# Kernel optimization log

Hardware: AMD Instinct MI355X
Metric: run time of the kernel (lower is better)

Reference implementation:

```python
import jax, jax.numpy as jnp
import numpy as np

ALPHA = 0.5            # conf['alpha'] hybrid mixing
MAX_TOP_ANT = 50       # conf['max_top_antecedents']
MAX_SPAN_WIDTH = 30


def bucket_distance(d):
    # util.bucket_distance: identity 0..4, then log2 buckets, clipped to [0, 9]
    logspace = jnp.floor(jnp.log2(jnp.maximum(d, 1).astype(jnp.float32))).astype(d.dtype) + 3
    return jnp.clip(jnp.where(d <= 4, d, logspace), 0, 9)


def setup_inputs() -> dict:
    key = jax.random.key(0)
    ks = jax.random.split(key, 16)
    W, D, K, F, H = 4096, 768, 768, 20, 1000
    SPAN = 3 * D                      # span_emb_size = 3 * bert_emb_size
    PAIR = 3 * SPAN + F               # pair_emb_size (use_features only)
    std = 0.02

    mention_doc = jax.random.normal(ks[0], (W, D), jnp.float32)
    mention_doc_one = jax.random.normal(ks[1], (W, D), jnp.float32)
    top_span_starts = jnp.sort(jax.random.randint(ks[2], (K,), 0, W - MAX_SPAN_WIDTH))
    widths = jax.random.randint(ks[3], (K,), 0, MAX_SPAN_WIDTH)
    top_span_ends = jnp.minimum(top_span_starts + widths, W - 1)
    top_span_mention_scores = jax.random.normal(ks[4], (K,), jnp.float32)

    return {
        "mention_doc": mention_doc,
        "mention_doc_one": mention_doc_one,
        "top_span_starts": top_span_starts,
        "top_span_ends": top_span_ends,
        "top_span_mention_scores": top_span_mention_scores,
        # mention_token_attn: Linear(D -> 1)
        "attn_w": jax.random.normal(ks[5], (D,), jnp.float32) * std,
        "attn_b": jnp.zeros((), jnp.float32),
        # coarse_bilinear: Linear(SPAN -> SPAN)
        "coarse_w": jax.random.normal(ks[6], (SPAN, SPAN), jnp.float32) * std,
        "coarse_b": jnp.zeros((SPAN,), jnp.float32),
        # emb_antecedent_distance_prior [10, F] + antecedent_distance_score_ffnn Linear(F -> 1)
        "dist_prior_emb": jax.random.normal(ks[7], (10, F), jnp.float32) * std,
        "dist_w": jax.random.normal(ks[8], (F,), jnp.float32) * std,
        "dist_b": jnp.zeros((), jnp.float32),
        # emb_top_antecedent_distance [10, F]
        "top_dist_emb": jax.random.normal(ks[9], (10, F), jnp.float32) * std,
        # coref_score_ffnn: Linear(PAIR -> H), ReLU, Linear(H -> 1)
        "coref_w1": jax.random.normal(ks[10], (PAIR, H), jnp.float32) * std,
        "coref_b1": jnp.zeros((H,), jnp.float32),
        "coref_w2": jax.random.normal(ks[11], (H,), jnp.float32) * std,
        "coref_b2": jnp.zeros((), jnp.float32),
    }


def reference(mention_doc, mention_doc_one, top_span_starts, top_span_ends,
              top_span_mention_scores, attn_w, attn_b, coarse_w, coarse_b,
              dist_prior_emb, dist_w, dist_b, top_dist_emb,
              coref_w1, coref_b1, coref_w2, coref_b2):
    W = mention_doc.shape[0]
    K = top_span_starts.shape[0]
    C = min(K, MAX_TOP_ANT)
    NEG_INF = jnp.float32(-1e30) * 0 - jnp.inf  # true -inf, matches torch.log(0.)

    # --- span embeddings: start / end / head-attention over hybrid doc ---
    start_emb = mention_doc[top_span_starts]                      # [K, D]
    end_emb = mention_doc[top_span_ends]                          # [K, D]
    hybrid = mention_doc * (1.0 - ALPHA) + mention_doc_one * ALPHA
    token_attn = hybrid @ attn_w + attn_b                         # [W]
    tok = jnp.arange(W)
    span_tok_mask = (tok[None, :] >= top_span_starts[:, None]) & \
                    (tok[None, :] <= top_span_ends[:, None])      # [K, W]
    attn_raw = jnp.where(span_tok_mask, token_attn[None, :], NEG_INF)
    attn_probs = jax.nn.softmax(attn_raw, axis=1)                 # [K, W]
    head_emb = attn_probs @ hybrid                                # [K, D]
    span_emb = jnp.concatenate([start_emb, end_emb, head_emb], axis=1)  # [K, 3D]

    # --- coarse (fast) pairwise scores ---
    rng = jnp.arange(K)
    ant_offsets = rng[:, None] - rng[None, :]                     # [K, K]
    ant_mask = ant_offsets >= 1
    pair_sum = top_span_mention_scores[:, None] + top_span_mention_scores[None, :]
    src = span_emb @ coarse_w + coarse_b                          # coarse_bilinear
    fast = pair_sum + src @ span_emb.T
    fast = jnp.where(ant_mask, fast, NEG_INF)                     # + log(mask)
    dist_score = dist_prior_emb @ dist_w + dist_b                 # [10]
    fast = fast + dist_score[bucket_distance(ant_offsets)]        # distance prior

    # --- top-k antecedent pruning ---
    top_fast, top_idx = jax.lax.top_k(fast, C)                    # [K, C]
    top_ant_offsets = jnp.take_along_axis(ant_offsets, top_idx, axis=1)

    # --- fine-grained pairwise FFNN scoring ---
    dist_emb = top_dist_emb[bucket_distance(top_ant_offsets)]     # [K, C, F]
    ant_emb = span_emb[top_idx]                                   # [K, C, 3D]
    tgt_emb = jnp.broadcast_to(span_emb[:, None, :], ant_emb.shape)
    sim_emb = span_emb[:, None, :] * ant_emb
    pair_emb = jnp.concatenate([tgt_emb, ant_emb, sim_emb, dist_emb], axis=-1)  # [K, C, PAIR]
    h = jax.nn.relu(jnp.einsum('kcp,ph->kch', pair_emb, coref_w1) + coref_b1)
    slow = jnp.einsum('kch,h->kc', h, coref_w2) + coref_b2        # [K, C]
    top_scores = slow + top_fast

    # dummy antecedent (epsilon) column of zeros
    return jnp.concatenate([jnp.zeros((K, 1), top_scores.dtype), top_scores], axis=1)
```

## Files before the change

kernel.cpp:

```cpp
#include <hip/hip_runtime.h>
#include <math.h>

#define WTOK 4096
#define DD   768
#define KK   768
#define SPAN 2304
#define HH   1000
#define CC   50
#define NPAD 1024
#define NBIG 4352

typedef __attribute__((ext_vector_type(8))) short bf16x8;
typedef __attribute__((ext_vector_type(4))) float f32x4;
typedef unsigned short ushort;
typedef unsigned int uint;

__device__ __forceinline__ int bucketd(int d) {
  int l = (d >= 1) ? (31 - __clz(d)) : 0;
  int v = (d <= 4) ? d : (l + 3);
  return min(max(v, 0), 9);
}
__device__ __forceinline__ ushort f2bf(float f) {
  uint u = __float_as_uint(f);
  return (ushort)((u + 0x7fffu + ((u >> 16) & 1u)) >> 16);
}
__device__ __forceinline__ uint pkmul_t(uint a, uint b) {
  float lo = __uint_as_float(a << 16) * __uint_as_float(b << 16);
  float hi = __uint_as_float(a & 0xffff0000u) * __uint_as_float(b & 0xffff0000u);
  return __builtin_amdgcn_perm(__float_as_uint(hi), __float_as_uint(lo), 0x07060302u);
}
__device__ __forceinline__ uint4 pkmul4(uint4 a, uint4 b) {
  uint4 r;
  r.x = pkmul_t(a.x, b.x); r.y = pkmul_t(a.y, b.y);
  r.z = pkmul_t(a.z, b.z); r.w = pkmul_t(a.w, b.w);
  return r;
}
__device__ __forceinline__ void dma16(const ushort* g, ushort* l) {
  __builtin_amdgcn_global_load_lds(
      (const __attribute__((address_space(1))) void*)g,
      (__attribute__((address_space(3))) void*)l, 16, 0, 0);
}

#define PB_COARSE 5184
#define PB_W 2304
#define PB_SETUP_BASE (PB_COARSE + 3 * PB_W)
#define PB_SLOW_BASE  (PB_SETUP_BASE + 40)
#define PB_TOTAL      (PB_SLOW_BASE + 150)

__global__ __launch_bounds__(256) void prep_k(
    const float* __restrict__ coarse_w, const float* __restrict__ W1,
    const float* __restrict__ dist_prior, const float* __restrict__ dist_w,
    const float* __restrict__ dist_b, const float* __restrict__ top_dist,
    ushort* __restrict__ BigT, ushort* __restrict__ W1simT,
    float* __restrict__ dist_score, float* __restrict__ Pdist,
    float* __restrict__ slow)
{
  int bid = blockIdx.x;
  int tid = threadIdx.x;
  if (bid >= PB_SLOW_BASE) {
    int t = (bid - PB_SLOW_BASE) * 256 + tid;
    if (t < KK * CC) slow[t] = 0.f;
    return;
  }
  if (bid >= PB_SETUP_BASE) {
    int t = (bid - PB_SETUP_BASE) * 256 + tid;
    if (t < 10) {
      float s = dist_b[0];
      for (int f = 0; f < 20; ++f) s += dist_prior[t * 20 + f] * dist_w[f];
      dist_score[t] = s;
    }
    if (t < 10 * HH) {
      int b = t / HH, h = t % HH;
      float s = 0.f;
      for (int f = 0; f < 20; ++f)
        s += top_dist[b * 20 + f] * W1[(long)(6912 + f) * HH + h];
      Pdist[t] = s;
    }
    return;
  }
  const float* in; int ldin, Cin, nbase, NBrows; ushort* out; int idx;
  int xt;
  if (bid < PB_COARSE) {
    idx = bid; in = coarse_w; ldin = SPAN; Cin = SPAN; nbase = 0;
    NBrows = NBIG; out = BigT; xt = SPAN / 32;
  } else {
    idx = bid - PB_COARSE;
    int region = idx / PB_W;
    idx = idx % PB_W;
    if (region == 0) { in = W1; nbase = 2304; NBrows = NBIG; out = BigT; }
    else if (region == 1) { in = W1 + (size_t)SPAN * HH; nbase = 3328; NBrows = NBIG; out = BigT; }
    else { in = W1 + (size_t)2 * SPAN * HH; nbase = 0; NBrows = NPAD; out = W1simT; }
    ldin = HH; Cin = HH; xt = NPAD / 32;
  }
  {
    int bx = idx % xt, by = idx / xt;
    __shared__ float tile[32][33];
    int n0 = bx * 32, p0 = by * 32;
    int tx = tid & 31, ty = tid >> 5;
    for (int i = ty; i < 32; i += 8) {
      int p = p0 + i, n = n0 + tx;
      tile[i][tx] = (n < Cin) ? in[(long)p * ldin + n] : 0.f;
    }
    __syncthreads();
    size_t slab = (size_t)(p0 >> 5) * NBrows * 32;
    for (int i = ty; i < 32; i += 8) {
      int n = n0 + i;
      out[slab + (size_t)(nbase + n) * 32 + tx] = f2bf(tile[tx][i]);
    }
  }
}

__global__ __launch_bounds__(256) void hybrid_attn_k(
    const float* __restrict__ doc, const float* __restrict__ doc1,
    const float* __restrict__ attn_w, const float* __restrict__ attn_b,
    float* __restrict__ hybrid, float* __restrict__ tok_attn)
{
  int w = blockIdx.x;
  int tid = threadIdx.x;
  float part = 0.f;
  for (int d = tid; d < DD; d += 256) {
    float h = 0.5f * doc[(long)w * DD + d] + 0.5f * doc1[(long)w * DD + d];
    hybrid[(long)w * DD + d] = h;
    part += h * attn_w[d];
  }
  for (int off = 32; off > 0; off >>= 1) part += __shfl_down(part, off, 64);
  __shared__ float ws4[4];
  if ((tid & 63) == 0) ws4[tid >> 6] = part;
  __syncthreads();
  if (tid == 0) tok_attn[w] = ws4[0] + ws4[1] + ws4[2] + ws4[3] + attn_b[0];
}

__global__ __launch_bounds__(256) void span_emb_k(
    const float* __restrict__ doc, const float* __restrict__ hybrid,
    const float* __restrict__ tok_attn, const int* __restrict__ starts,
    const int* __restrict__ ends, ushort* __restrict__ se_bf)
{
  int k = blockIdx.x;
  int s = starts[k], e = ends[k];
  int len = e - s + 1;
  int tid = threadIdx.x;
  __shared__ float p_s[32];
  if (tid < 32) {
    float v = (tid < len) ? tok_attn[s + tid] : -INFINITY;
    float m = v;
    for (int msk = 16; msk >= 1; msk >>= 1) m = fmaxf(m, __shfl_xor(m, msk, 32));
    float pe = (tid < len) ? expf(v - m) : 0.f;
    float Z = pe;
    for (int msk = 16; msk >= 1; msk >>= 1) Z += __shfl_xor(Z, msk, 32);
    p_s[tid] = pe / Z;
  }
  __syncthreads();
  for (int d = tid; d < DD; d += 256) {
    float h = 0.f;
    for (int t = 0; t < len; ++t) h += p_s[t] * hybrid[(long)(s + t) * DD + d];
    se_bf[(long)k * SPAN + d]          = f2bf(doc[(long)s * DD + d]);
    se_bf[(long)k * SPAN + DD + d]     = f2bf(doc[(long)e * DD + d]);
    se_bf[(long)k * SPAN + 2 * DD + d] = f2bf(h);
  }
}

__global__ __launch_bounds__(256) void gemm_combined_k(
    const ushort* __restrict__ A, const ushort* __restrict__ B,
    const float* __restrict__ coarse_b, const float* __restrict__ b1,
    ushort* __restrict__ src_bf, float* __restrict__ Ptgt,
    float* __restrict__ Pant)
{
  __shared__ __align__(16) ushort As[64 * 40];
  __shared__ __align__(16) ushort Bs[128 * 32];
  int tid = threadIdx.x;
  int m0 = blockIdx.x * 64, n0 = blockIdx.y * 128;
  int lane = tid & 63, wid = tid >> 6;
  int quad = lane >> 4, lr = lane & 15;
  int wm = (wid & 1) << 5, wn = (wid >> 1) << 6;
  int arow = tid >> 2, aq = tid & 3;
  int gofs[2];
#pragma unroll
  for (int t = 0; t < 2; ++t) {
    int S = t * 256 + tid;
    int r = S >> 2, p = S & 3;
    int q = p ^ ((r >> 1) & 3);
    gofs[t] = (n0 + r) * 32 + q * 8;
  }
  f32x4 acc[2][4] = {};
  for (int k0 = 0; k0 < SPAN; k0 += 32) {
    uint4 a0 = *(const uint4*)(A + (size_t)(m0 + arow) * SPAN + k0 + aq * 8);
    __syncthreads();
    const ushort* sb = B + (size_t)(k0 >> 5) * (NBIG * 32);
    dma16(sb + gofs[0], &Bs[(size_t)(0 * 256 + tid) * 8]);
    dma16(sb + gofs[1], &Bs[(size_t)(1 * 256 + tid) * 8]);
    *(uint4*)&As[arow * 40 + aq * 8] = a0;
    __syncthreads();
    bf16x8 af[2], bfr[4];
#pragma unroll
    for (int mi = 0; mi < 2; ++mi)
      af[mi] = *(const bf16x8*)&As[(wm + mi * 16 + lr) * 40 + quad * 8];
#pragma unroll
    for (int ni = 0; ni < 4; ++ni) {
      int r = wn + ni * 16 + lr;
      int p = quad ^ ((r >> 1) & 3);
      bfr[ni] = *(const bf16x8*)&Bs[r * 32 + p * 8];
    }
#pragma unroll
    for (int mi = 0; mi < 2; ++mi)
#pragma unroll
      for (int ni = 0; ni < 4; ++ni)
        acc[mi][ni] = __builtin_amdgcn_mfma_f32_16x16x32_bf16(
            af[mi], bfr[ni], acc[mi][ni], 0, 0, 0);
  }
#pragma unroll
  for (int mi = 0; mi < 2; ++mi)
#pragma unroll
    for (int ni = 0; ni < 4; ++ni) {
      f32x4 c = acc[mi][ni];
#pragma unroll
      for (int reg = 0; reg < 4; ++reg) {
        int gm = m0 + wm + mi * 16 + quad * 4 + reg;
        int g = n0 + wn + ni * 16 + lr;
        float v = c[reg];
        if (g < 2304) {
          src_bf[(size_t)gm * SPAN + g] = f2bf(v + coarse_b[g]);
        } else if (g < 3328) {
          int n = g - 2304;
          if (n < HH) Ptgt[(size_t)gm * HH + n] = v + b1[n];
        } else {
          int n = g - 3328;
          if (n < HH) Pant[(size_t)gm * HH + n] = v;
        }
      }
    }
}

__global__ __launch_bounds__(256) void gemm_fast_k(
    const ushort* __restrict__ A, const ushort* __restrict__ B,
    const float* __restrict__ ms, const float* __restrict__ dist_score,
    float* __restrict__ fast)
{
  __shared__ __align__(16) ushort As[64 * 40];
  __shared__ __align__(16) ushort Bs[64 * 40];
  int tid = threadIdx.x;
  int m0 = blockIdx.x * 64, n0 = blockIdx.y * 64;
  int lane = tid & 63, wid = tid >> 6;
  int quad = lane >> 4, lr = lane & 15;
  int wm = (wid & 1) << 5, wn = (wid >> 1) << 5;
  int row = tid >> 2, aq = tid & 3;
  const ushort* ga = A + (size_t)(m0 + row) * SPAN + aq * 8;
  const ushort* gb = B + (size_t)(n0 + row) * SPAN + aq * 8;
  f32x4 acc[2][2] = {};
  for (int k0 = 0; k0 < SPAN; k0 += 32) {
    uint4 a0 = *(const uint4*)(ga + k0);
    uint4 b0 = *(const uint4*)(gb + k0);
    __syncthreads();
    *(uint4*)&As[row * 40 + aq * 8] = a0;
    *(uint4*)&Bs[row * 40 + aq * 8] = b0;
    __syncthreads();
    bf16x8 af[2], bfr[2];
#pragma unroll
    for (int mi = 0; mi < 2; ++mi)
      af[mi] = *(const bf16x8*)&As[(wm + mi * 16 + lr) * 40 + quad * 8];
#pragma unroll
    for (int ni = 0; ni < 2; ++ni)
      bfr[ni] = *(const bf16x8*)&Bs[(wn + ni * 16 + lr) * 40 + quad * 8];
#pragma unroll
    for (int mi = 0; mi < 2; ++mi)
#pragma unroll
      for (int ni = 0; ni < 2; ++ni)
        acc[mi][ni] = __builtin_amdgcn_mfma_f32_16x16x32_bf16(
            af[mi], bfr[ni], acc[mi][ni], 0, 0, 0);
  }
#pragma unroll
  for (int mi = 0; mi < 2; ++mi)
#pragma unroll
    for (int ni = 0; ni < 2; ++ni) {
      f32x4 c = acc[mi][ni];
#pragma unroll
      for (int reg = 0; reg < 4; ++reg) {
        int gm = m0 + wm + mi * 16 + quad * 4 + reg;
        int gn = n0 + wn + ni * 16 + lr;
        float v;
        if (gn < gm) {
          v = c[reg] + ms[gm] + ms[gn] + dist_score[bucketd(gm - gn)];
        } else {
          v = -INFINITY;
        }
        fast[(size_t)gm * KK + gn] = v;
      }
    }
}

__global__ __launch_bounds__(256) void topk_k(
    const float* __restrict__ fast, float* __restrict__ top_fast,
    int* __restrict__ row_j, int* __restrict__ row_bucket)
{
  __shared__ float vals[KK];
  __shared__ float wbv[4];
  __shared__ int wbi[4];
  int k = blockIdx.x;
  int tid = threadIdx.x;
  for (int j = tid; j < KK; j += 256) vals[j] = fast[(long)k * KK + j];
  __syncthreads();
  const float NANF = __uint_as_float(0x7fc00000u);
  for (int it = 0; it < CC; ++it) {
    float bv = -INFINITY;
    int bi = 1 << 30;
    for (int j = tid; j < KK; j += 256) {
      float v = vals[j];
      if (v > bv || (v == bv && j < bi)) { bv = v; bi = j; }
    }
    for (int off = 32; off > 0; off >>= 1) {
      float ov = __shfl_down(bv, off, 64);
      int oi = __shfl_down(bi, off, 64);
      if (ov > bv || (ov == bv && oi < bi)) { bv = ov; bi = oi; }
    }
    if ((tid & 63) == 0) { wbv[tid >> 6] = bv; wbi[tid >> 6] = bi; }
    __syncthreads();
    if (tid == 0) {
      for (int w = 1; w < 4; ++w) {
        float ov = wbv[w]; int oi = wbi[w];
        if (ov > bv || (ov == bv && oi < bi)) { bv = ov; bi = oi; }
      }
      int r = k * CC + it;
      top_fast[r] = bv;
      row_j[r] = bi;
      row_bucket[r] = bucketd(k - bi);
      vals[bi] = NANF;
    }
    __syncthreads();
  }
}

__global__ __launch_bounds__(512, 4) void pair_mfma_k(
    const ushort* __restrict__ se_bf, const ushort* __restrict__ W1simT,
    const int* __restrict__ row_j, const int* __restrict__ row_bucket,
    const float* __restrict__ Ptgt, const float* __restrict__ Pant,
    const float* __restrict__ Pdist, const float* __restrict__ w2,
    float* __restrict__ slow)
{
  __shared__ __align__(16) ushort As[2][128 * 32];
  __shared__ __align__(16) ushort Bs[2][256 * 32];
  __shared__ int ks_s[128];
  __shared__ int js_s[128];
  __shared__ int bk_s[128];
  int tid = threadIdx.x;
  int m0 = blockIdx.x * 128, n0 = blockIdx.y * 256;
  if (tid < 128) {
    int r = m0 + tid;
    ks_s[tid] = r / CC;
    js_s[tid] = row_j[r];
    bk_s[tid] = row_bucket[r];
  }
  __syncthreads();
  int lane = tid & 63, wid = tid >> 6;
  int quad = lane >> 4, lr = lane & 15;
  int wm = (wid & 3) << 5;
  int wn = (wid >> 2) << 7;
  int ar0 = tid >> 2, aq = tid & 3;
  const ushort* pk0 = se_bf + (size_t)ks_s[ar0] * SPAN + aq * 8;
  const ushort* pj0 = se_bf + (size_t)js_s[ar0] * SPAN + aq * 8;
  int gofs[2];
#pragma unroll
  for (int t = 0; t < 2; ++t) {
    int S = t * 512 + tid;
    int r = S >> 2, p = S & 3;
    int q = p ^ ((r >> 1) & 3);
    gofs[t] = (n0 + r) * 32 + q * 8;
  }
  int awi0 = ar0 * 32 + (aq ^ ((ar0 >> 1) & 3)) * 8;

  {
    uint4 ka0 = *(const uint4*)(pk0);
    uint4 ja0 = *(const uint4*)(pj0);
#pragma unroll
    for (int t = 0; t < 2; ++t)
      dma16(W1simT + gofs[t], &Bs[0][(size_t)(t * 512 + tid) * 8]);
    *(uint4*)&As[0][awi0] = pkmul4(ka0, ja0);
  }
  __syncthreads();

  f32x4 acc[2][8] = {};
  for (int k0 = 0; k0 < SPAN; k0 += 32) {
    int buf = (k0 >> 5) & 1, nb = buf ^ 1;
    bool more = (k0 + 32) < SPAN;
    int k1 = more ? k0 + 32 : k0;
    uint4 ka0 = *(const uint4*)(pk0 + k1);
    uint4 ja0 = *(const uint4*)(pj0 + k1);
    if (more) {
      const ushort* sb = W1simT + (size_t)(k1 >> 5) * (NPAD * 32);
#pragma unroll
      for (int t = 0; t < 2; ++t)
        dma16(sb + gofs[t], &Bs[nb][(size_t)(t * 512 + tid) * 8]);
    }
    bf16x8 af[2], bfr[8];
#pragma unroll
    for (int mi = 0; mi < 2; ++mi) {
      int r = wm + mi * 16 + lr;
      int p = quad ^ ((r >> 1) & 3);
      af[mi] = *(const bf16x8*)&As[buf][r * 32 + p * 8];
    }
#pragma unroll
    for (int ni = 0; ni < 8; ++ni) {
      int r = wn + ni * 16 + lr;
      int p = quad ^ ((r >> 1) & 3);
      bfr[ni] = *(const bf16x8*)&Bs[buf][r * 32 + p * 8];
    }
#pragma unroll
    for (int ni = 0; ni < 8; ++ni)
#pragma unroll
      for (int mi = 0; mi < 2; ++mi)
        acc[mi][ni] = __builtin_amdgcn_mfma_f32_16x16x32_bf16(
            af[mi], bfr[ni], acc[mi][ni], 0, 0, 0);
    if (more) {
      *(uint4*)&As[nb][awi0] = pkmul4(ka0, ja0);
    }
    __syncthreads();
  }
  int nn[8]; float w2r[8]; bool nv[8];
#pragma unroll
  for (int ni = 0; ni < 8; ++ni) {
    nn[ni] = n0 + wn + ni * 16 + lr;
    nv[ni] = nn[ni] < HH;
    w2r[ni] = nv[ni] ? w2[nn[ni]] : 0.f;
  }
#pragma unroll
  for (int mi = 0; mi < 2; ++mi) {
#pragma unroll
    for (int reg = 0; reg < 4; ++reg) {
      int rl = wm + mi * 16 + quad * 4 + reg;
      int kk = ks_s[rl], jj = js_s[rl], bb = bk_s[rl];
      float s = 0.f;
#pragma unroll
      for (int ni = 0; ni < 8; ++ni) {
        if (nv[ni]) {
          float h = acc[mi][ni][reg] + Ptgt[(size_t)kk * HH + nn[ni]] +
                    Pant[(size_t)jj * HH + nn[ni]] +
                    Pdist[(size_t)bb * HH + nn[ni]];
          s += fmaxf(h, 0.f) * w2r[ni];
        }
      }
      s += __shfl_xor(s, 1); s += __shfl_xor(s, 2);
      s += __shfl_xor(s, 4); s += __shfl_xor(s, 8);
      if (lr == 0) atomicAdd(&slow[m0 + rl], s);
    }
  }
}

__global__ void finalize_k(const float* __restrict__ slow,
                           const float* __restrict__ top_fast,
                           const float* __restrict__ b2, float* __restrict__ out)
{
  int t = blockIdx.x * 256 + threadIdx.x;
  if (t >= KK * (CC + 1)) return;
  int k = t / (CC + 1), col = t % (CC + 1);
  if (col == 0) {
    out[t] = 0.f;
  } else {
    int r = k * CC + col - 1;
    float v = slow[r] + b2[0] + top_fast[r];
    if (!isfinite(v)) v = -1.0e30f;
    out[t] = v;
  }
}

extern "C" void kernel_launch(void* const* d_in, const int* in_sizes, int n_in,
                              void* d_out, int out_size, void* d_ws, size_t ws_size,
                              hipStream_t stream)
{
  const float* doc        = (const float*)d_in[0];
  const float* doc1       = (const float*)d_in[1];
  const int*   starts     = (const int*)d_in[2];
  const int*   ends       = (const int*)d_in[3];
  const float* ms         = (const float*)d_in[4];
  const float* attn_w     = (const float*)d_in[5];
  const float* attn_b     = (const float*)d_in[6];
  const float* coarse_w   = (const float*)d_in[7];
  const float* coarse_b   = (const float*)d_in[8];
  const float* dist_prior = (const float*)d_in[9];
  const float* dist_w     = (const float*)d_in[10];
  const float* dist_b     = (const float*)d_in[11];
  const float* top_dist   = (const float*)d_in[12];
  const float* W1         = (const float*)d_in[13];
  const float* b1         = (const float*)d_in[14];
  const float* w2         = (const float*)d_in[15];
  const float* b2         = (const float*)d_in[16];
  float* out = (float*)d_out;

  char* ws = (char*)d_ws;
  size_t off = 0;
  auto alloc = [&](size_t bytes) { void* p = ws + off; off = (off + bytes + 1023) & ~(size_t)1023; return p; };
  float*  hybrid     = (float*)alloc((size_t)WTOK * DD * 4);
  float*  tok_attn   = (float*)alloc((size_t)WTOK * 4);
  ushort* se_bf      = (ushort*)alloc((size_t)KK * SPAN * 2 + 4096);
  ushort* src_bf     = (ushort*)alloc((size_t)KK * SPAN * 2 + 4096);
  float*  fast       = (float*)alloc((size_t)KK * KK * 4);
  float*  Ptgt       = (float*)alloc((size_t)KK * HH * 4);
  float*  Pant       = (float*)alloc((size_t)KK * HH * 4);
  float*  Pdist      = (float*)alloc((size_t)10 * HH * 4);
  float*  dist_score = (float*)alloc(64);
  float*  top_fast   = (float*)alloc((size_t)KK * CC * 4);
  int*    row_j      = (int*)alloc((size_t)KK * CC * 4);
  int*    row_bucket = (int*)alloc((size_t)KK * CC * 4);
  float*  slow       = (float*)alloc((size_t)KK * CC * 4);
  ushort* BigT       = (ushort*)alloc((size_t)NBIG * SPAN * 2 + 4096);
  ushort* W1simT     = (ushort*)alloc((size_t)NPAD * SPAN * 2 + 4096);
  (void)ws_size; (void)in_sizes; (void)n_in; (void)out_size;

  prep_k<<<PB_TOTAL, 256, 0, stream>>>(coarse_w, W1, dist_prior, dist_w,
                                       dist_b, top_dist, BigT, W1simT,
                                       dist_score, Pdist, slow);
  hybrid_attn_k<<<WTOK, 256, 0, stream>>>(doc, doc1, attn_w, attn_b, hybrid, tok_attn);
  span_emb_k<<<KK, 256, 0, stream>>>(doc, hybrid, tok_attn, starts, ends, se_bf);
  {
    dim3 g(KK / 64, NBIG / 128);
    gemm_combined_k<<<g, 256, 0, stream>>>(se_bf, BigT, coarse_b, b1,
                                           src_bf, Ptgt, Pant);
  }
  {
    dim3 g(KK / 64, KK / 64);
    gemm_fast_k<<<g, 256, 0, stream>>>(src_bf, se_bf, ms, dist_score, fast);
  }
  topk_k<<<KK, 256, 0, stream>>>(fast, top_fast, row_j, row_bucket);
  {
    dim3 g((KK * CC) / 128, NPAD / 256);
    pair_mfma_k<<<g, 512, 0, stream>>>(se_bf, W1simT, row_j, row_bucket,
                                       Ptgt, Pant, Pdist, w2, slow);
  }
  finalize_k<<<(KK * (CC + 1) + 255) / 256, 256, 0, stream>>>(slow, top_fast, b2, out);
}
```

Measured before the change: 522.9 us.

## Double-buffer GEMM tiles, fuse hybrid attn into prep, wave-per-row top-k

The hybrid attention kernel is folded into prep_k as extra blocks, saving one launch and letting that work run alongside the weight transposes. Both bf16 GEMMs gain double-buffered LDS tiles, so the next k-slice load overlaps the MFMAs and only one barrier remains per iteration. Top-k now gives each row to a single wavefront. Each lane packs its values and indices into 64-bit order-preserving keys held in registers and does max reductions through 64-bit shuffles, which removes the LDS traffic and block barriers of the old per-row loop. The cost is more LDS for the GEMMs and more registers for the key arrays.

```diff
diff --git a/kernel.cpp b/kernel.cpp
--- a/kernel.cpp
+++ b/kernel.cpp
@@ -14,6 +14,7 @@
 typedef __attribute__((ext_vector_type(4))) float f32x4;
 typedef unsigned short ushort;
 typedef unsigned int uint;
+typedef unsigned long long u64;
 
 __device__ __forceinline__ int bucketd(int d) {
   int l = (d >= 1) ? (31 - __clz(d)) : 0;
@@ -40,23 +41,48 @@
       (const __attribute__((address_space(1))) void*)g,
       (__attribute__((address_space(3))) void*)l, 16, 0, 0);
 }
+__device__ __forceinline__ u64 shflx64(u64 v, int msk) {
+  uint lo = (uint)v, hi = (uint)(v >> 32);
+  lo = (uint)__shfl_xor((int)lo, msk, 64);
+  hi = (uint)__shfl_xor((int)hi, msk, 64);
+  return ((u64)hi << 32) | lo;
+}
 
 #define PB_COARSE 5184
 #define PB_W 2304
 #define PB_SETUP_BASE (PB_COARSE + 3 * PB_W)
 #define PB_SLOW_BASE  (PB_SETUP_BASE + 40)
-#define PB_TOTAL      (PB_SLOW_BASE + 150)
+#define PB_HYB_BASE   (PB_SLOW_BASE + 150)
+#define PB_TOTAL      (PB_HYB_BASE + WTOK)
 
 __global__ __launch_bounds__(256) void prep_k(
     const float* __restrict__ coarse_w, const float* __restrict__ W1,
     const float* __restrict__ dist_prior, const float* __restrict__ dist_w,
     const float* __restrict__ dist_b, const float* __restrict__ top_dist,
+    const float* __restrict__ doc, const float* __restrict__ doc1,
+    const float* __restrict__ attn_w, const float* __restrict__ attn_b,
     ushort* __restrict__ BigT, ushort* __restrict__ W1simT,
     float* __restrict__ dist_score, float* __restrict__ Pdist,
-    float* __restrict__ slow)
+    float* __restrict__ slow, float* __restrict__ hybrid,
+    float* __restrict__ tok_attn)
 {
   int bid = blockIdx.x;
   int tid = threadIdx.x;
+  if (bid >= PB_HYB_BASE) {
+    int w = bid - PB_HYB_BASE;
+    float part = 0.f;
+    for (int d = tid; d < DD; d += 256) {
+      float h = 0.5f * doc[(long)w * DD + d] + 0.5f * doc1[(long)w * DD + d];
+      hybrid[(long)w * DD + d] = h;
+      part += h * attn_w[d];
+    }
+    for (int off = 32; off > 0; off >>= 1) part += __shfl_down(part, off, 64);
+    __shared__ float ws4[4];
+    if ((tid & 63) == 0) ws4[tid >> 6] = part;
+    __syncthreads();
+    if (tid == 0) tok_attn[w] = ws4[0] + ws4[1] + ws4[2] + ws4[3] + attn_b[0];
+    return;
+  }
   if (bid >= PB_SLOW_BASE) {
     int t = (bid - PB_SLOW_BASE) * 256 + tid;
     if (t < KK * CC) slow[t] = 0.f;
@@ -110,26 +136,6 @@
   }
 }
 
-__global__ __launch_bounds__(256) void hybrid_attn_k(
-    const float* __restrict__ doc, const float* __restrict__ doc1,
-    const float* __restrict__ attn_w, const float* __restrict__ attn_b,
-    float* __restrict__ hybrid, float* __restrict__ tok_attn)
-{
-  int w = blockIdx.x;
-  int tid = threadIdx.x;
-  float part = 0.f;
-  for (int d = tid; d < DD; d += 256) {
-    float h = 0.5f * doc[(long)w * DD + d] + 0.5f * doc1[(long)w * DD + d];
-    hybrid[(long)w * DD + d] = h;
-    part += h * attn_w[d];
-  }
-  for (int off = 32; off > 0; off >>= 1) part += __shfl_down(part, off, 64);
-  __shared__ float ws4[4];
-  if ((tid & 63) == 0) ws4[tid >> 6] = part;
-  __syncthreads();
-  if (tid == 0) tok_attn[w] = ws4[0] + ws4[1] + ws4[2] + ws4[3] + attn_b[0];
-}
-
 __global__ __launch_bounds__(256) void span_emb_k(
     const float* __restrict__ doc, const float* __restrict__ hybrid,
     const float* __restrict__ tok_attn, const int* __restrict__ starts,
@@ -165,8 +171,8 @@
     ushort* __restrict__ src_bf, float* __restrict__ Ptgt,
     float* __restrict__ Pant)
 {
-  __shared__ __align__(16) ushort As[64 * 40];
-  __shared__ __align__(16) ushort Bs[128 * 32];
+  __shared__ __align__(16) ushort As[2][64 * 40];
+  __shared__ __align__(16) ushort Bs[2][128 * 32];
   int tid = threadIdx.x;
   int m0 = blockIdx.x * 64, n0 = blockIdx.y * 128;
   int lane = tid & 63, wid = tid >> 6;
@@ -181,24 +187,34 @@
     int q = p ^ ((r >> 1) & 3);
     gofs[t] = (n0 + r) * 32 + q * 8;
   }
+  const ushort* ga = A + (size_t)(m0 + arow) * SPAN + aq * 8;
+  {
+    uint4 a0 = *(const uint4*)(ga);
+    dma16(B + gofs[0], &Bs[0][(size_t)(0 * 256 + tid) * 8]);
+    dma16(B + gofs[1], &Bs[0][(size_t)(1 * 256 + tid) * 8]);
+    *(uint4*)&As[0][arow * 40 + aq * 8] = a0;
+  }
+  __syncthreads();
   f32x4 acc[2][4] = {};
   for (int k0 = 0; k0 < SPAN; k0 += 32) {
-    uint4 a0 = *(const uint4*)(A + (size_t)(m0 + arow) * SPAN + k0 + aq * 8);
-    __syncthreads();
-    const ushort* sb = B + (size_t)(k0 >> 5) * (NBIG * 32);
-    dma16(sb + gofs[0], &Bs[(size_t)(0 * 256 + tid) * 8]);
-    dma16(sb + gofs[1], &Bs[(size_t)(1 * 256 + tid) * 8]);
-    *(uint4*)&As[arow * 40 + aq * 8] = a0;
-    __syncthreads();
+    int buf = (k0 >> 5) & 1, nb = buf ^ 1;
+    bool more = (k0 + 32) < SPAN;
+    uint4 a_nxt;
+    if (more) {
+      a_nxt = *(const uint4*)(ga + k0 + 32);
+      const ushort* sb = B + (size_t)((k0 >> 5) + 1) * (NBIG * 32);
+      dma16(sb + gofs[0], &Bs[nb][(size_t)(0 * 256 + tid) * 8]);
+      dma16(sb + gofs[1], &Bs[nb][(size_t)(1 * 256 + tid) * 8]);
+    }
     bf16x8 af[2], bfr[4];
 #pragma unroll
     for (int mi = 0; mi < 2; ++mi)
-      af[mi] = *(const bf16x8*)&As[(wm + mi * 16 + lr) * 40 + quad * 8];
+      af[mi] = *(const bf16x8*)&As[buf][(wm + mi * 16 + lr) * 40 + quad * 8];
 #pragma unroll
     for (int ni = 0; ni < 4; ++ni) {
       int r = wn + ni * 16 + lr;
       int p = quad ^ ((r >> 1) & 3);
-      bfr[ni] = *(const bf16x8*)&Bs[r * 32 + p * 8];
+      bfr[ni] = *(const bf16x8*)&Bs[buf][r * 32 + p * 8];
     }
 #pragma unroll
     for (int mi = 0; mi < 2; ++mi)
@@ -206,6 +222,8 @@
       for (int ni = 0; ni < 4; ++ni)
         acc[mi][ni] = __builtin_amdgcn_mfma_f32_16x16x32_bf16(
             af[mi], bfr[ni], acc[mi][ni], 0, 0, 0);
+    if (more) *(uint4*)&As[nb][arow * 40 + aq * 8] = a_nxt;
+    __syncthreads();
   }
 #pragma unroll
   for (int mi = 0; mi < 2; ++mi)
@@ -235,8 +253,8 @@
     const float* __restrict__ ms, const float* __restrict__ dist_score,
     float* __restrict__ fast)
 {
-  __shared__ __align__(16) ushort As[64 * 40];
-  __shared__ __align__(16) ushort Bs[64 * 40];
+  __shared__ __align__(16) ushort As[2][64 * 40];
+  __shared__ __align__(16) ushort Bs[2][64 * 40];
   int tid = threadIdx.x;
   int m0 = blockIdx.x * 64, n0 = blockIdx.y * 64;
   int lane = tid & 63, wid = tid >> 6;
@@ -245,27 +263,40 @@
   int row = tid >> 2, aq = tid & 3;
   const ushort* ga = A + (size_t)(m0 + row) * SPAN + aq * 8;
   const ushort* gb = B + (size_t)(n0 + row) * SPAN + aq * 8;
+  {
+    uint4 a0 = *(const uint4*)(ga);
+    uint4 b0 = *(const uint4*)(gb);
+    *(uint4*)&As[0][row * 40 + aq * 8] = a0;
+    *(uint4*)&Bs[0][row * 40 + aq * 8] = b0;
+  }
+  __syncthreads();
   f32x4 acc[2][2] = {};
   for (int k0 = 0; k0 < SPAN; k0 += 32) {
-    uint4 a0 = *(const uint4*)(ga + k0);
-    uint4 b0 = *(const uint4*)(gb + k0);
-    __syncthreads();
-    *(uint4*)&As[row * 40 + aq * 8] = a0;
-    *(uint4*)&Bs[row * 40 + aq * 8] = b0;
-    __syncthreads();
+    int buf = (k0 >> 5) & 1, nb = buf ^ 1;
+    bool more = (k0 + 32) < SPAN;
+    uint4 a_nxt, b_nxt;
+    if (more) {
+      a_nxt = *(const uint4*)(ga + k0 + 32);
+      b_nxt = *(const uint4*)(gb + k0 + 32);
+    }
     bf16x8 af[2], bfr[2];
 #pragma unroll
     for (int mi = 0; mi < 2; ++mi)
-      af[mi] = *(const bf16x8*)&As[(wm + mi * 16 + lr) * 40 + quad * 8];
+      af[mi] = *(const bf16x8*)&As[buf][(wm + mi * 16 + lr) * 40 + quad * 8];
 #pragma unroll
     for (int ni = 0; ni < 2; ++ni)
-      bfr[ni] = *(const bf16x8*)&Bs[(wn + ni * 16 + lr) * 40 + quad * 8];
+      bfr[ni] = *(const bf16x8*)&Bs[buf][(wn + ni * 16 + lr) * 40 + quad * 8];
 #pragma unroll
     for (int mi = 0; mi < 2; ++mi)
 #pragma unroll
       for (int ni = 0; ni < 2; ++ni)
         acc[mi][ni] = __builtin_amdgcn_mfma_f32_16x16x32_bf16(
             af[mi], bfr[ni], acc[mi][ni], 0, 0, 0);
+    if (more) {
+      *(uint4*)&As[nb][row * 40 + aq * 8] = a_nxt;
+      *(uint4*)&Bs[nb][row * 40 + aq * 8] = b_nxt;
+    }
+    __syncthreads();
   }
 #pragma unroll
   for (int mi = 0; mi < 2; ++mi)
@@ -291,40 +322,35 @@
     const float* __restrict__ fast, float* __restrict__ top_fast,
     int* __restrict__ row_j, int* __restrict__ row_bucket)
 {
-  __shared__ float vals[KK];
-  __shared__ float wbv[4];
-  __shared__ int wbi[4];
-  int k = blockIdx.x;
-  int tid = threadIdx.x;
-  for (int j = tid; j < KK; j += 256) vals[j] = fast[(long)k * KK + j];
-  __syncthreads();
-  const float NANF = __uint_as_float(0x7fc00000u);
+  int lane = threadIdx.x & 63;
+  int k = blockIdx.x * 4 + (threadIdx.x >> 6);
+  u64 key[12];
+#pragma unroll
+  for (int i = 0; i < 12; ++i) {
+    int j = lane + i * 64;
+    uint u = __float_as_uint(fast[(size_t)k * KK + j]);
+    uint s = (u & 0x80000000u) ? ~u : (u | 0x80000000u);
+    key[i] = ((u64)s << 10) | (u64)(1023 - j);
+  }
   for (int it = 0; it < CC; ++it) {
-    float bv = -INFINITY;
-    int bi = 1 << 30;
-    for (int j = tid; j < KK; j += 256) {
-      float v = vals[j];
-      if (v > bv || (v == bv && j < bi)) { bv = v; bi = j; }
-    }
-    for (int off = 32; off > 0; off >>= 1) {
-      float ov = __shfl_down(bv, off, 64);
-      int oi = __shfl_down(bi, off, 64);
-      if (ov > bv || (ov == bv && oi < bi)) { bv = ov; bi = oi; }
-    }
-    if ((tid & 63) == 0) { wbv[tid >> 6] = bv; wbi[tid >> 6] = bi; }
-    __syncthreads();
-    if (tid == 0) {
-      for (int w = 1; w < 4; ++w) {
-        float ov = wbv[w]; int oi = wbi[w];
-        if (ov > bv || (ov == bv && oi < bi)) { bv = ov; bi = oi; }
-      }
+    u64 gm = key[0];
+#pragma unroll
+    for (int i = 1; i < 12; ++i) gm = (key[i] > gm) ? key[i] : gm;
+    for (int msk = 32; msk > 0; msk >>= 1) {
+      u64 o = shflx64(gm, msk);
+      gm = (o > gm) ? o : gm;
+    }
+#pragma unroll
+    for (int i = 0; i < 12; ++i) if (key[i] == gm) key[i] = 0;
+    if (lane == 0) {
+      uint s = (uint)(gm >> 10);
+      uint u = (s & 0x80000000u) ? (s & 0x7fffffffu) : ~s;
+      int j = 1023 - (int)(gm & 1023u);
       int r = k * CC + it;
-      top_fast[r] = bv;
-      row_j[r] = bi;
-      row_bucket[r] = bucketd(k - bi);
-      vals[bi] = NANF;
-    }
-    __syncthreads();
+      top_fast[r] = __uint_as_float(u);
+      row_j[r] = j;
+      row_bucket[r] = bucketd(k - j);
+    }
   }
 }
 
@@ -504,9 +530,9 @@
   (void)ws_size; (void)in_sizes; (void)n_in; (void)out_size;
 
   prep_k<<<PB_TOTAL, 256, 0, stream>>>(coarse_w, W1, dist_prior, dist_w,
-                                       dist_b, top_dist, BigT, W1simT,
-                                       dist_score, Pdist, slow);
-  hybrid_attn_k<<<WTOK, 256, 0, stream>>>(doc, doc1, attn_w, attn_b, hybrid, tok_attn);
+                                       dist_b, top_dist, doc, doc1, attn_w,
+                                       attn_b, BigT, W1simT, dist_score,
+                                       Pdist, slow, hybrid, tok_attn);
   span_emb_k<<<KK, 256, 0, stream>>>(doc, hybrid, tok_attn, starts, ends, se_bf);
   {
     dim3 g(KK / 64, NBIG / 128);
@@ -517,7 +543,7 @@
     dim3 g(KK / 64, KK / 64);
     gemm_fast_k<<<g, 256, 0, stream>>>(src_bf, se_bf, ms, dist_score, fast);
   }
-  topk_k<<<KK, 256, 0, stream>>>(fast, top_fast, row_j, row_bucket);
+  topk_k<<<KK / 4, 256, 0, stream>>>(fast, top_fast, row_j, row_bucket);
   {
     dim3 g((KK * CC) / 128, NPAD / 256);
     pair_mfma_k<<<g, 512, 0, stream>>>(se_bf, W1simT, row_j, row_bucket,
```

Result: faster. 479.3 us (-8.3%).
